# Kernel optimization log

Measured on AMD Instinct MI355X. Metric: run time of the kernel, lower is better.

## Reference

```python
import jax, jax.numpy as jnp
import numpy as np

SCALE = 0.1    # BinarizeConv2dSDP scale factor
BN_EPS = 1e-5

def _binarize(x):
    # straight-through sign binarization (STE): forward = sign(x), grad = identity
    return x + jax.lax.stop_gradient(jnp.sign(x) - x)

def _bin_conv3x3(x, w, stride=1):
    # binarize activations and weights; per-output-channel weight scaling alpha = mean|w|
    a_b = _binarize(x)
    alpha = jnp.mean(jnp.abs(w), axis=(1, 2, 3))          # [Cout]
    w_b = _binarize(w)
    y = jax.lax.conv_general_dilated(
        a_b, w_b, window_strides=(stride, stride), padding=((1, 1), (1, 1)),
        dimension_numbers=('NCHW', 'OIHW', 'NCHW'))
    return y * (SCALE * alpha)[None, :, None, None]

def _batchnorm(x, gamma, beta):
    mu = jnp.mean(x, axis=(0, 2, 3), keepdims=True)
    var = jnp.var(x, axis=(0, 2, 3), keepdims=True)
    xh = (x - mu) * jax.lax.rsqrt(var + BN_EPS)
    return xh * gamma[None, :, None, None] + beta[None, :, None, None]

def _prelu(x, a):
    return jnp.where(x >= 0, x, a.reshape(()) * x)

def setup_inputs() -> dict:
    key = jax.random.key(0)
    ks = jax.random.split(key, 5)
    B, C, H, W = 64, 256, 28, 28
    return {
        'x': jax.random.normal(ks[0], (B, C, H, W), jnp.float32),
        'conv1_w': jax.random.normal(ks[1], (C, C, 3, 3), jnp.float32) * 0.05,
        'conv2_w': jax.random.normal(ks[2], (C, C, 3, 3), jnp.float32) * 0.05,
        'bn1_gamma': jnp.ones((C,), jnp.float32),
        'bn1_beta': jnp.zeros((C,), jnp.float32),
        'bn2_gamma': jnp.ones((C,), jnp.float32),
        'bn2_beta': jnp.zeros((C,), jnp.float32),
        'prelu1_a': jnp.full((1,), 0.25, jnp.float32),
        'prelu2_a': jnp.full((1,), 0.25, jnp.float32),
    }

def reference(x, conv1_w, conv2_w, bn1_gamma, bn1_beta, bn2_gamma, bn2_beta, prelu1_a, prelu2_a):
    residual = x
    out = _bin_conv3x3(x, conv1_w, stride=1)
    out = _batchnorm(out, bn1_gamma, bn1_beta)
    out = out + residual
    out = _prelu(out, prelu1_a)
    residual = out
    out = _bin_conv3x3(out, conv2_w, stride=1)
    out = _batchnorm(out, bn2_gamma, bn2_beta)
    out = out + residual
    out = _prelu(out, prelu2_a)
    return out
```

## Files before the change

kernel.cpp:

```cpp
#include <hip/hip_runtime.h>
#include <cstdint>

#define NB 64
#define NC 256
#define HW 784
#define NPIX (NB*HW)
#define NELEM ((size_t)NB*NC*HW)

#define HALO_ROWS 122
#define A_BYTES (HALO_ROWS*256)
#define ZERO_OFF A_BYTES

typedef int v4i  __attribute__((ext_vector_type(4)));
typedef int v16i __attribute__((ext_vector_type(16)));

union U16 { signed char b[16]; int4 v; };

__global__ __launch_bounds__(256) void alpha_k(
    const float* __restrict__ w1, const float* __restrict__ w2,
    float* __restrict__ al1, float* __restrict__ al2) {
  int blk = blockIdx.x;
  int conv = blk >> 8, cout = blk & 255;
  const float* w = (conv ? w2 : w1) + (size_t)cout * 2304;
  int t = threadIdx.x;
  float s = 0.0f;
  for (int i = t; i < 2304; i += 256) s += fabsf(w[i]);
  __shared__ float red[256];
  red[t] = s;
  __syncthreads();
  for (int st = 128; st > 0; st >>= 1) {
    if (t < st) red[t] += red[t + st];
    __syncthreads();
  }
  if (t == 0) (conv ? al2 : al1)[cout] = red[0] / 2304.0f;
}

__global__ __launch_bounds__(256) void wfrag_k(
    const float* __restrict__ w1, const float* __restrict__ w2,
    signed char* __restrict__ Wf1, signed char* __restrict__ Wf2) {
  int bi = blockIdx.x;
  int conv = bi / 72, r = bi % 72, tap = r >> 3, cg = r & 7;
  const float* w = conv ? w2 : w1;
  signed char* Wf = conv ? Wf2 : Wf1;
  int t = threadIdx.x;
  for (int e = t; e < 512; e += 256) {
    int c = e >> 6, lane = e & 63;
    int cout = cg * 32 + (lane & 31);
    int cin0 = c * 32 + (lane >> 5) * 16;
    U16 u;
#pragma unroll
    for (int bb = 0; bb < 16; ++bb) {
      float v = w[((size_t)cout * 256 + cin0 + bb) * 9 + tap];
      u.b[bb] = v > 0.f ? 1 : (v < 0.f ? -1 : 0);
    }
    *(int4*)(Wf + ((((size_t)tap * 8 + c) * 8 + cg) * 64 + lane) * 16) = u.v;
  }
}

__global__ __launch_bounds__(256) void pack_x(
    const float* __restrict__ in, signed char* __restrict__ A) {
  __shared__ float tile[256 * 33];
  int t = threadIdx.x;
  int P0 = blockIdx.x * 32;
  int pl = t & 31, c0 = t >> 5;
  int P = P0 + pl;
  int b = P / HW, hw = P - b * HW;
  size_t base = (size_t)b * (NC * HW) + (size_t)c0 * HW + hw;
#pragma unroll
  for (int i = 0; i < 32; ++i)
    tile[(i * 8 + c0) * 33 + pl] = in[base + (size_t)i * 8 * HW];
  __syncthreads();
  int g = t >> 4, pls = t & 15;
#pragma unroll
  for (int ph = 0; ph < 2; ++ph) {
    int pp = ph * 16 + pls;
    U16 u;
#pragma unroll
    for (int bb = 0; bb < 16; ++bb) {
      float v = tile[(g * 16 + bb) * 33 + pp];
      u.b[bb] = v > 0.f ? 1 : (v < 0.f ? -1 : 0);
    }
    *(int4*)(A + (size_t)(P0 + pp) * 256 + g * 16) = u.v;
  }
}

__global__ __launch_bounds__(256, 4) void conv_mfma(
    const signed char* __restrict__ A, const signed char* __restrict__ Wf,
    short* __restrict__ dotb,
    int* __restrict__ pd, int* __restrict__ pq) {
  __shared__ signed char As[A_BYTES + 256];
  int t = threadIdx.x;
  int lane = t & 63, wid = t >> 6;
  int mblk = blockIdx.x;
  int p0 = mblk * 64;
  int khalf = lane >> 5;

  {
    const signed char* src = A + (size_t)(p0 - 29) * 256;
#pragma unroll
    for (int i = 0; i < 8; ++i) {
      int off = i * 4096 + t * 16;
      if (off < A_BYTES) {
        int4 d = *(const int4*)(src + off);
        int r = off >> 8, g = (off >> 4) & 15;
        int gs = g ^ ((r + 3) & 15);
        *(int4*)(As + r * 256 + gs * 16) = d;
      }
    }
    if (t < 16) { int4 z = {0, 0, 0, 0}; *(int4*)(As + ZERO_OFF + t * 16) = z; }
  }

  int prow[2], hh[2], ww[2];
#pragma unroll
  for (int i = 0; i < 2; ++i) {
    int p = p0 + i * 32 + (lane & 31);
    prow[i] = p;
    int hw = p % HW;
    hh[i] = hw / 28;
    ww[i] = hw - hh[i] * 28;
  }
  __syncthreads();

  v16i acc[2][2];
  {
    v16i z = {0};
    acc[0][0] = z; acc[0][1] = z; acc[1][0] = z; acc[1][1] = z;
  }

  const signed char* wlane = Wf + ((size_t)(wid * 2) * 64 + lane) * 16;

  for (int tap = 0; tap < 9; ++tap) {
    int ky = (tap >= 3) + (tap >= 6);
    int kx = tap - 3 * ky;
    int dlt = (ky - 1) * 28 + (kx - 1);
    int rb0, rb1, kk0, kk1;
    {
      int hp = hh[0] + ky - 1, wp = ww[0] + kx - 1;
      bool val = ((unsigned)hp < 28u) && ((unsigned)wp < 28u);
      int pr = prow[0] + dlt;
      rb0 = val ? (pr - (p0 - 29)) * 256 : ZERO_OFF;
      kk0 = val ? ((pr & 15) << 4) : 0;
      hp = hh[1] + ky - 1; wp = ww[1] + kx - 1;
      val = ((unsigned)hp < 28u) && ((unsigned)wp < 28u);
      pr = prow[1] + dlt;
      rb1 = val ? (pr - (p0 - 29)) * 256 : ZERO_OFF;
      kk1 = val ? ((pr & 15) << 4) : 0;
    }
    const signed char* wt = wlane + (size_t)tap * 65536;
#pragma unroll
    for (int c = 0; c < 8; ++c) {
      int gl4 = (c * 2 + khalf) << 4;
      v4i a0 = *(const v4i*)(As + rb0 + (gl4 ^ kk0));
      v4i a1 = *(const v4i*)(As + rb1 + (gl4 ^ kk1));
      v4i w0 = *(const v4i*)(wt + c * 8192);
      v4i w1 = *(const v4i*)(wt + c * 8192 + 1024);
      acc[0][0] = __builtin_amdgcn_mfma_i32_32x32x32_i8(a0, w0, acc[0][0], 0, 0, 0);
      acc[0][1] = __builtin_amdgcn_mfma_i32_32x32x32_i8(a0, w1, acc[0][1], 0, 0, 0);
      acc[1][0] = __builtin_amdgcn_mfma_i32_32x32x32_i8(a1, w0, acc[1][0], 0, 0, 0);
      acc[1][1] = __builtin_amdgcn_mfma_i32_32x32x32_i8(a1, w1, acc[1][1], 0, 0, 0);
    }
  }

#pragma unroll
  for (int j = 0; j < 2; ++j) {
    int s = 0, sq = 0;
#pragma unroll
    for (int i = 0; i < 2; ++i)
#pragma unroll
      for (int q = 0; q < 16; ++q) {
        int v = acc[i][j][q];
        s += v; sq += v * v;
      }
    s += __shfl_xor(s, 32); sq += __shfl_xor(sq, 32);
    if (lane < 32) {
      pd[mblk * 256 + wid * 64 + j * 32 + lane] = s;
      pq[mblk * 256 + wid * 64 + j * 32 + lane] = sq;
    }
  }

#pragma unroll
  for (int i = 0; i < 2; ++i) {
    int pr = p0 + i * 32 + 4 * khalf;
#pragma unroll
    for (int j = 0; j < 2; ++j) {
      int cb = wid * 64 + j * 32;
#pragma unroll
      for (int q = 0; q < 16; ++q) {
        int row = pr + (q & 3) + 8 * (q >> 2);
        dotb[(size_t)row * 256 + cb + (lane & 31)] = (short)acc[i][j][q];
      }
    }
  }
}

__global__ __launch_bounds__(256) void bn_finalize(
    const int* __restrict__ pd, const int* __restrict__ pq,
    const float* __restrict__ alpha, const float* __restrict__ gamma,
    const float* __restrict__ beta, float* __restrict__ scale,
    float* __restrict__ shift) {
  int c = blockIdx.x, t = threadIdx.x;
  long long D = 0, D2 = 0;
  for (int r = t; r < 784; r += 256) {
    D  += (long long)pd[r * 256 + c];
    D2 += (long long)pq[r * 256 + c];
  }
  __shared__ long long rd[256], rq[256];
  rd[t] = D; rq[t] = D2;
  __syncthreads();
  for (int st = 128; st > 0; st >>= 1) {
    if (t < st) { rd[t] += rd[t + st]; rq[t] += rq[t + st]; }
    __syncthreads();
  }
  if (t == 0) {
    float sc = 0.1f * alpha[c];
    const float invN = 1.0f / (float)(NB * HW);
    float md  = (float)rd[0] * invN;
    float ex2 = (float)rq[0] * invN;
    float var = sc * sc * (ex2 - md * md);
    float rs = rsqrtf(var + 1e-5f);
    float g = gamma[c];
    scale[c] = rs * g * sc;
    shift[c] = beta[c] - sc * md * rs * g;
  }
}

__global__ __launch_bounds__(256) void bn_mid(
    const short* __restrict__ dot, const float* __restrict__ x,
    const float* __restrict__ scale, const float* __restrict__ shift,
    const float* __restrict__ pa, float* __restrict__ a1,
    signed char* __restrict__ A) {
  __shared__ short rawd[32 * 264];
  __shared__ float tile[256 * 33];
  __shared__ float ssc[256], ssh[256];
  int t = threadIdx.x;
  int P0 = blockIdx.x * 32;
  ssc[t] = scale[t]; ssh[t] = shift[t];
  float ap = pa[0];
#pragma unroll
  for (int i = 0; i < 4; ++i) {
    int idx = i * 256 + t;
    int pl = idx >> 5, g = idx & 31;
    int4 d = *(const int4*)(dot + (size_t)(P0 + pl) * 256 + g * 8);
    *(int4*)(&rawd[pl * 264 + g * 8]) = d;
  }
  __syncthreads();
  int pl = t & 31, c0 = t >> 5;
  int P = P0 + pl;
  int b = P / HW, hw = P - b * HW;
  size_t base = (size_t)b * (NC * HW) + (size_t)c0 * HW + hw;
#pragma unroll
  for (int i = 0; i < 32; ++i) {
    int c = i * 8 + c0;
    size_t addr = base + (size_t)i * 8 * HW;
    float d = (float)rawd[pl * 264 + c];
    float v = fmaf(d, ssc[c], ssh[c]) + x[addr];
    float o = v >= 0.0f ? v : ap * v;
    a1[addr] = o;
    tile[c * 33 + pl] = o;
  }
  __syncthreads();
  int g = t >> 4, pls = t & 15;
#pragma unroll
  for (int ph = 0; ph < 2; ++ph) {
    int pp = ph * 16 + pls;
    U16 u;
#pragma unroll
    for (int bb = 0; bb < 16; ++bb) {
      float v = tile[(g * 16 + bb) * 33 + pp];
      u.b[bb] = v > 0.f ? 1 : (v < 0.f ? -1 : 0);
    }
    *(int4*)(A + (size_t)(P0 + pp) * 256 + g * 16) = u.v;
  }
}

__global__ __launch_bounds__(256) void bn_fin_apply(
    const short* __restrict__ dot, const float* __restrict__ res,
    const float* __restrict__ scale, const float* __restrict__ shift,
    const float* __restrict__ pa, float* __restrict__ out) {
  __shared__ short rawd[32 * 264];
  __shared__ float ssc[256], ssh[256];
  int t = threadIdx.x;
  int P0 = blockIdx.x * 32;
  ssc[t] = scale[t]; ssh[t] = shift[t];
  float ap = pa[0];
#pragma unroll
  for (int i = 0; i < 4; ++i) {
    int idx = i * 256 + t;
    int pl = idx >> 5, g = idx & 31;
    int4 d = *(const int4*)(dot + (size_t)(P0 + pl) * 256 + g * 8);
    *(int4*)(&rawd[pl * 264 + g * 8]) = d;
  }
  __syncthreads();
  int pl = t & 31, c0 = t >> 5;
  int P = P0 + pl;
  int b = P / HW, hw = P - b * HW;
  size_t base = (size_t)b * (NC * HW) + (size_t)c0 * HW + hw;
#pragma unroll
  for (int i = 0; i < 32; ++i) {
    int c = i * 8 + c0;
    size_t addr = base + (size_t)i * 8 * HW;
    float d = (float)rawd[pl * 264 + c];
    float v = fmaf(d, ssc[c], ssh[c]) + res[addr];
    out[addr] = v >= 0.0f ? v : ap * v;
  }
}

extern "C" void kernel_launch(void* const* d_in, const int* in_sizes, int n_in,
                              void* d_out, int out_size, void* d_ws, size_t ws_size,
                              hipStream_t stream) {
  const float* x   = (const float*)d_in[0];
  const float* w1  = (const float*)d_in[1];
  const float* w2  = (const float*)d_in[2];
  const float* g1  = (const float*)d_in[3];
  const float* b1  = (const float*)d_in[4];
  const float* g2  = (const float*)d_in[5];
  const float* b2  = (const float*)d_in[6];
  const float* pa1 = (const float*)d_in[7];
  const float* pa2 = (const float*)d_in[8];
  float* out = (float*)d_out;

  char* ws = (char*)d_ws;
  short*       dotb = (short*)ws;       ws += (size_t)NPIX * 256 * 2;
  signed char* Abuf = (signed char*)ws; ws += (size_t)NPIX * 256;
  signed char* Wf1  = (signed char*)ws; ws += 589824;
  signed char* Wf2  = (signed char*)ws; ws += 589824;
  float*       a1   = (float*)ws;       ws += NELEM * 4;
  int* pd1 = (int*)ws; ws += 784 * 256 * 4;
  int* pq1 = (int*)ws; ws += 784 * 256 * 4;
  int* pd2 = (int*)ws; ws += 784 * 256 * 4;
  int* pq2 = (int*)ws; ws += 784 * 256 * 4;
  float* alpha1 = (float*)ws; ws += 1024;
  float* alpha2 = (float*)ws; ws += 1024;
  float* scale1 = (float*)ws; ws += 1024;
  float* shift1 = (float*)ws; ws += 1024;
  float* scale2 = (float*)ws; ws += 1024;
  float* shift2 = (float*)ws; ws += 1024;

  alpha_k<<<512, 256, 0, stream>>>(w1, w2, alpha1, alpha2);
  wfrag_k<<<144, 256, 0, stream>>>(w1, w2, Wf1, Wf2);
  pack_x<<<NPIX / 32, 256, 0, stream>>>(x, Abuf);

  conv_mfma<<<784, 256, 0, stream>>>(Abuf, Wf1, dotb, pd1, pq1);
  bn_finalize<<<256, 256, 0, stream>>>(pd1, pq1, alpha1, g1, b1, scale1, shift1);
  bn_mid<<<NPIX / 32, 256, 0, stream>>>(dotb, x, scale1, shift1, pa1, a1, Abuf);

  conv_mfma<<<784, 256, 0, stream>>>(Abuf, Wf2, dotb, pd2, pq2);
  bn_finalize<<<256, 256, 0, stream>>>(pd2, pq2, alpha2, g2, b2, scale2, shift2);
  bn_fin_apply<<<NPIX / 32, 256, 0, stream>>>(dotb, a1, scale2, shift2, pa2, out);
}
```

Before: 166.3 us.

## Stage conv weights through double-buffered LDS with register prefetch

```diff
diff --git a/kernel.cpp b/kernel.cpp
--- a/kernel.cpp
+++ b/kernel.cpp
@@ -10,6 +10,9 @@
 #define HALO_ROWS 122
 #define A_BYTES (HALO_ROWS*256)
 #define ZERO_OFF A_BYTES
+#define W_LDS_OFF (A_BYTES + 256)
+#define W_BUF_SZ 16384
+#define CONV_LDS (W_LDS_OFF + 2*W_BUF_SZ)
 
 typedef int v4i  __attribute__((ext_vector_type(4)));
 typedef int v16i __attribute__((ext_vector_type(16)));
@@ -84,11 +87,14 @@
   }
 }
 
-__global__ __launch_bounds__(256, 4) void conv_mfma(
+__global__ __launch_bounds__(256, 2) void conv_mfma(
     const signed char* __restrict__ A, const signed char* __restrict__ Wf,
     short* __restrict__ dotb,
     int* __restrict__ pd, int* __restrict__ pq) {
-  __shared__ signed char As[A_BYTES + 256];
+  __shared__ signed char smem[CONV_LDS];
+  signed char* As = smem;
+  signed char* Wlds = smem + W_LDS_OFF;
+
   int t = threadIdx.x;
   int lane = t & 63, wid = t >> 6;
   int mblk = blockIdx.x;
@@ -109,6 +115,14 @@
     }
     if (t < 16) { int4 z = {0, 0, 0, 0}; *(int4*)(As + ZERO_OFF + t * 16) = z; }
   }
+  {
+#pragma unroll
+    for (int i = 0; i < 4; ++i) {
+      int off = i * 4096 + t * 16;
+      int4 d = *(const int4*)(Wf + off);
+      *(int4*)(Wlds + off) = d;
+    }
+  }
 
   int prow[2], hh[2], ww[2];
 #pragma unroll
@@ -127,14 +141,17 @@
     acc[0][0] = z; acc[0][1] = z; acc[1][0] = z; acc[1][1] = z;
   }
 
-  const signed char* wlane = Wf + ((size_t)(wid * 2) * 64 + lane) * 16;
-
-  for (int tap = 0; tap < 9; ++tap) {
-    int ky = (tap >= 3) + (tap >= 6);
-    int kx = tap - 3 * ky;
-    int dlt = (ky - 1) * 28 + (kx - 1);
-    int rb0, rb1, kk0, kk1;
-    {
+  int rb0 = 0, rb1 = 0, kk0 = 0, kk1 = 0;
+  const int wrd_off = wid * 2048 + lane * 16;
+
+  for (int ph = 0; ph < 36; ++ph) {
+    const int cur = ph & 1;
+
+    if ((ph & 3) == 0) {
+      const int tap = ph >> 2;
+      const int ky = (tap >= 3) + (tap >= 6);
+      const int kx = tap - 3 * ky;
+      const int dlt = (ky - 1) * 28 + (kx - 1);
       int hp = hh[0] + ky - 1, wp = ww[0] + kx - 1;
       bool val = ((unsigned)hp < 28u) && ((unsigned)wp < 28u);
       int pr = prow[0] + dlt;
@@ -146,19 +163,39 @@
       rb1 = val ? (pr - (p0 - 29)) * 256 : ZERO_OFF;
       kk1 = val ? ((pr & 15) << 4) : 0;
     }
-    const signed char* wt = wlane + (size_t)tap * 65536;
-#pragma unroll
-    for (int c = 0; c < 8; ++c) {
-      int gl4 = (c * 2 + khalf) << 4;
+
+    int4 wreg0, wreg1, wreg2, wreg3;
+    if (ph < 35) {
+      const signed char* wsrc = Wf + (size_t)(ph + 1) * 16384 + t * 16;
+      wreg0 = *(const int4*)(wsrc);
+      wreg1 = *(const int4*)(wsrc + 4096);
+      wreg2 = *(const int4*)(wsrc + 8192);
+      wreg3 = *(const int4*)(wsrc + 12288);
+    }
+
+    const signed char* wbuf = Wlds + cur * W_BUF_SZ;
+#pragma unroll
+    for (int cl = 0; cl < 2; ++cl) {
+      const int chunk = (ph & 3) * 2 + cl;
+      const int gl4 = ((chunk * 2 + khalf) << 4);
       v4i a0 = *(const v4i*)(As + rb0 + (gl4 ^ kk0));
       v4i a1 = *(const v4i*)(As + rb1 + (gl4 ^ kk1));
-      v4i w0 = *(const v4i*)(wt + c * 8192);
-      v4i w1 = *(const v4i*)(wt + c * 8192 + 1024);
+      v4i w0 = *(const v4i*)(wbuf + cl * 8192 + wrd_off);
+      v4i w1 = *(const v4i*)(wbuf + cl * 8192 + wrd_off + 1024);
       acc[0][0] = __builtin_amdgcn_mfma_i32_32x32x32_i8(a0, w0, acc[0][0], 0, 0, 0);
       acc[0][1] = __builtin_amdgcn_mfma_i32_32x32x32_i8(a0, w1, acc[0][1], 0, 0, 0);
       acc[1][0] = __builtin_amdgcn_mfma_i32_32x32x32_i8(a1, w0, acc[1][0], 0, 0, 0);
       acc[1][1] = __builtin_amdgcn_mfma_i32_32x32x32_i8(a1, w1, acc[1][1], 0, 0, 0);
     }
+
+    if (ph < 35) {
+      signed char* wdst = Wlds + (cur ^ 1) * W_BUF_SZ + t * 16;
+      *(int4*)(wdst)         = wreg0;
+      *(int4*)(wdst + 4096)  = wreg1;
+      *(int4*)(wdst + 8192)  = wreg2;
+      *(int4*)(wdst + 12288) = wreg3;
+    }
+    __syncthreads();
   }
 
 #pragma unroll
```

New measurement: 196.2 us. 17.9% more time.
